# Kernel optimization log

Measured on AMD Instinct MI355X. Metric: run time of the kernel, lower is better.

The kernel has to match this reference:

```python
import jax, jax.numpy as jnp
import numpy as np

D = 256        # model_dim
E = 4          # num_experts
H = 8          # attention heads
L = 8          # layers
P = 4          # patch size
IMG = 128
B = 8
NUM_CLASSES = 10
T = (IMG // P) ** 2  # 1024 tokens


def _ln(x, g, b):
    mu = jnp.mean(x, -1, keepdims=True)
    var = jnp.mean((x - mu) ** 2, -1, keepdims=True)
    return (x - mu) * jax.lax.rsqrt(var + 1e-5) * g + b


def setup_inputs() -> dict:
    key = jax.random.key(0)
    ks = jax.random.split(key, 24)
    n = lambda k, s, sc=0.02: jax.random.normal(k, s, jnp.float32) * sc
    return {
        "x": jax.random.normal(ks[0], (B, 3, IMG, IMG), jnp.float32),
        "patch_w": n(ks[1], (D, 3, P, P), 0.1),
        "patch_b": n(ks[2], (D,), 0.01),
        "pos_emb": n(ks[3], (1, T, D), 0.02),
        "router_w": n(ks[4], (E, D), 0.05),
        "router_b": n(ks[5], (E,), 0.01),
        "ln1_g": jnp.ones((L, D), jnp.float32),
        "ln1_b": jnp.zeros((L, D), jnp.float32),
        "q_w": n(ks[6], (L, D, D), 0.05),
        "q_b": n(ks[7], (L, D), 0.01),
        "k_w": n(ks[8], (L, D, D), 0.05),
        "k_b": n(ks[9], (L, D), 0.01),
        "v_w": n(ks[10], (L, D, D), 0.05),
        "v_b": n(ks[11], (L, D), 0.01),
        "o_w": n(ks[12], (L, D, D), 0.05),
        "o_b": n(ks[13], (L, D), 0.01),
        "ln2_g": jnp.ones((L, D), jnp.float32),
        "ln2_b": jnp.zeros((L, D), jnp.float32),
        "l1_w": n(ks[14], (L, 4 * D, D), 0.05),
        "l1_b": n(ks[15], (L, 4 * D), 0.01),
        "l2_w": n(ks[16], (L, D, 4 * D), 0.05),
        "l2_b": n(ks[17], (L, D), 0.01),
        "head_w": n(ks[18], (NUM_CLASSES, D), 0.05),
        "head_b": n(ks[19], (NUM_CLASSES,), 0.01),
        "alpha": jnp.full((1,), 0.5, jnp.float32),
    }


def reference(x, patch_w, patch_b, pos_emb, router_w, router_b, ln1_g, ln1_b,
              q_w, q_b, k_w, k_b, v_w, v_b, o_w, o_b, ln2_g, ln2_b,
              l1_w, l1_b, l2_w, l2_b, head_w, head_b, alpha):
    b = x.shape[0]
    # patch embed: Conv2d(3, D, P, stride=P)
    h = jax.lax.conv_general_dilated(x, patch_w, (P, P), 'VALID',
                                     dimension_numbers=('NCHW', 'OIHW', 'NCHW'))
    h = h + patch_b[None, :, None, None]
    tok = h.reshape(b, D, -1).transpose(0, 2, 1) + pos_emb   # [B,T,D]
    t = tok.shape[1]
    n_per = t // E  # uniform capacity: floor(T * 1/E)
    raw_prob = jax.nn.softmax(tok @ router_w.T + router_b, axis=-1)  # [B,T,E]
    # greedy routing: expert e takes top n_per of remaining tokens, rows zeroed after
    prob = raw_prob
    bidx = jnp.arange(b)[:, None]
    blocks, pblocks = [], []
    for e in range(E):
        _, idx = jax.lax.top_k(prob[:, :, e], n_per)            # [B,n_per]
        blocks.append(jnp.take_along_axis(tok, idx[:, :, None], axis=1))
        pblocks.append(jnp.take_along_axis(raw_prob, idx[:, :, None], axis=1))
        sel = jnp.zeros((b, t), prob.dtype).at[bidx, idx].set(1.0)
        prob = prob * (1.0 - sel)[:, :, None]
    xs = jnp.concatenate(blocks, axis=1)    # [B,T,D] expert-sorted
    rp = jnp.concatenate(pblocks, axis=1)   # [B,T,E]

    widths = [D // 2 ** e for e in range(E)]  # [256,128,64,32]
    scale = D ** -0.5                         # note: model_dim, not head_dim
    dh = D // H
    for l in range(L):
        # ---- nested-expert MHSA ----
        xn = _ln(xs, ln1_g[l], ln1_b[l])
        qs, ks_, vs = [], [], []
        for e in range(E):
            m = widths[e]
            blk = xn[:, e * n_per:(e + 1) * n_per, :m]
            qs.append(blk @ q_w[l][:, :m].T + q_b[l])
            ks_.append(blk @ k_w[l][:, :m].T + k_b[l])
            vs.append(blk @ v_w[l][:, :m].T + v_b[l])
        q = jnp.concatenate(qs, 1).reshape(b, t, H, dh).transpose(0, 2, 1, 3)
        k = jnp.concatenate(ks_, 1).reshape(b, t, H, dh).transpose(0, 2, 1, 3)
        v = jnp.concatenate(vs, 1).reshape(b, t, H, dh).transpose(0, 2, 1, 3)
        attn = jax.nn.softmax(jnp.einsum('bhqd,bhkd->bhqk', q, k) * scale, axis=-1)
        ao = jnp.einsum('bhqk,bhkd->bhqd', attn, v).transpose(0, 2, 1, 3).reshape(b, t, D)
        outs = []
        for e in range(E):
            m = widths[e]
            sl = slice(e * n_per, (e + 1) * n_per)
            o = ao[:, sl, :m] @ o_w[l][:m, :m].T + o_b[l][:m]
            o = jnp.pad(o, ((0, 0), (0, 0), (0, D - m)))
            outs.append(o + xs[:, sl, :])
        xs = jnp.concatenate(outs, 1)
        # ---- nested-expert MLP ----
        xn = _ln(xs, ln2_g[l], ln2_b[l])
        outs = []
        for e in range(E):
            m = widths[e]
            sl = slice(e * n_per, (e + 1) * n_per)
            blk = xn[:, sl, :m]
            inner = jax.nn.gelu(blk @ l1_w[l][:, :m].T + l1_b[l], approximate=False)
            outer = inner @ l2_w[l][:m, :].T + l2_b[l][:m]
            outer = jnp.pad(outer, ((0, 0), (0, 0), (0, D - m)))
            sf = (alpha[0] * rp[:, sl, e] + 1.0)[:, :, None]
            outs.append(xs[:, sl, :] + sf * outer)
        xs = jnp.concatenate(outs, 1)
    # classification head: mean pool + linear
    return jnp.mean(xs, axis=1) @ head_w.T + head_b
```

## Files before the change

### kernel.cpp

```cpp
#include <hip/hip_runtime.h>
#include <math.h>

#define D 256
#define E 4
#define H 8
#define LYR 8
#define IMG 128
#define BB 8
#define NC 10
#define T 1024
#define NPER 256
#define DH 32
#define D4 1024

using bf16x8 = __attribute__((ext_vector_type(8))) __bf16;
using bf16x4 = __attribute__((ext_vector_type(4))) __bf16;
using f32x4  = __attribute__((ext_vector_type(4))) float;

#define MFMA16(a, b, c) __builtin_amdgcn_mfma_f32_16x16x32_bf16((a), (b), (c), 0, 0, 0)

__device__ __forceinline__ void gload16(const void* g, void* l) {
    __builtin_amdgcn_global_load_lds(
        (const __attribute__((address_space(1))) void*)g,
        (__attribute__((address_space(3))) void*)l, 16, 0, 0);
}

__global__ void cast6(const float* __restrict__ s0, const float* __restrict__ s1,
                      const float* __restrict__ s2, const float* __restrict__ s3,
                      const float* __restrict__ s4, const float* __restrict__ s5,
                      __bf16* __restrict__ d0, __bf16* __restrict__ d1,
                      __bf16* __restrict__ d2, __bf16* __restrict__ d3,
                      __bf16* __restrict__ d4, __bf16* __restrict__ d5) {
    const long A4 = (long)LYR * D * D / 4;
    const long W4 = (long)LYR * D4 * D / 4;
    long i = (long)blockIdx.x * 256 + threadIdx.x;
    const float* s; __bf16* d; long off;
    if (i < 4 * A4) {
        int w = (int)(i / A4); off = i - (long)w * A4;
        s = w == 0 ? s0 : w == 1 ? s1 : w == 2 ? s2 : s3;
        d = w == 0 ? d0 : w == 1 ? d1 : w == 2 ? d2 : d3;
    } else {
        long j = i - 4 * A4;
        int w = (int)(j / W4); off = j - (long)w * W4;
        s = w ? s5 : s4; d = w ? d5 : d4;
    }
    float4 v = ((const float4*)s)[off];
    bf16x4 o;
    o[0] = (__bf16)v.x; o[1] = (__bf16)v.y; o[2] = (__bf16)v.z; o[3] = (__bf16)v.w;
    ((bf16x4*)d)[off] = o;
}

__global__ void patch_router(const float* __restrict__ x, const float* __restrict__ pw,
                             const float* __restrict__ pb, const float* __restrict__ pos,
                             const float* __restrict__ rw, const float* __restrict__ rb,
                             float* __restrict__ tok, float* __restrict__ rawp) {
    int t = blockIdx.x, b = blockIdx.y, d = threadIdx.x;
    __shared__ float sx[48];
    __shared__ float srow[D];
    __shared__ float slog[4];
    int ph = t >> 5, pwc = t & 31;
    if (d < 48) {
        int c = d >> 4, ij = d & 15, i = ij >> 2, j = ij & 3;
        sx[d] = x[(((long)b * 3 + c) * IMG + (ph * 4 + i)) * IMG + (pwc * 4 + j)];
    }
    __syncthreads();
    float acc = pb[d];
    #pragma unroll
    for (int kk = 0; kk < 48; ++kk) acc += sx[kk] * pw[d * 48 + kk];
    float val = acc + pos[(long)t * D + d];
    tok[((long)b * T + t) * D + d] = val;
    srow[d] = val;
    __syncthreads();
    int wv = d >> 6, lane = d & 63;
    float a = 0.f;
    for (int c = lane; c < D; c += 64) a += srow[c] * rw[wv * D + c];
    for (int off = 32; off; off >>= 1) a += __shfl_down(a, off);
    if (lane == 0) slog[wv] = a + rb[wv];
    __syncthreads();
    if (d == 0) {
        float l0 = slog[0], l1 = slog[1], l2 = slog[2], l3 = slog[3];
        float mx = fmaxf(fmaxf(l0, l1), fmaxf(l2, l3));
        float e0 = __expf(l0 - mx), e1 = __expf(l1 - mx), e2 = __expf(l2 - mx), e3 = __expf(l3 - mx);
        float inv = 1.0f / (e0 + e1 + e2 + e3);
        long row = (long)b * T + t;
        rawp[row * 4 + 0] = e0 * inv;
        rawp[row * 4 + 1] = e1 * inv;
        rawp[row * 4 + 2] = e2 * inv;
        rawp[row * 4 + 3] = e3 * inv;
    }
}

__global__ __launch_bounds__(1024) void route_topk(const float* __restrict__ rawp,
                                                   int* __restrict__ perm,
                                                   float* __restrict__ rpsel) {
    int b = blockIdx.x, tid = threadIdx.x;
    int lane = tid & 63, wv = tid >> 6;
    __shared__ unsigned hist[256];
    __shared__ unsigned long long ball[16];
    __shared__ int sb_bin, sb_rem;
    bool assigned = false;
    for (int e = 0; e < E; ++e) {
        float v = rawp[((long)b * T + tid) * E + e];
        unsigned key = assigned ? 0u : __float_as_uint(v);
        unsigned prefix = 0;
        int rem = NPER;
        #pragma unroll
        for (int pass = 3; pass >= 0; --pass) {
            int shift = pass * 8;
            if (tid < 256) hist[tid] = 0;
            __syncthreads();
            bool active = (pass == 3) || ((key >> (shift + 8)) == prefix);
            if (active) atomicAdd(&hist[(key >> shift) & 255], 1u);
            __syncthreads();
            if (tid < 64) {
                unsigned c[4], psum = 0;
                #pragma unroll
                for (int u = 0; u < 4; ++u) { c[u] = hist[tid * 4 + u]; psum += c[u]; }
                unsigned suf = psum;
                #pragma unroll
                for (int off = 1; off < 64; off <<= 1) {
                    unsigned o = __shfl_down(suf, off);
                    if (tid + off < 64) suf += o;
                }
                unsigned El = suf - psum;
                if (El < (unsigned)rem && (unsigned)rem <= suf) {
                    unsigned cab = El;
                    #pragma unroll
                    for (int u = 3; u >= 0; --u) {
                        if ((unsigned)rem > cab && (unsigned)rem <= cab + c[u]) {
                            sb_bin = tid * 4 + u;
                            sb_rem = (int)((unsigned)rem - cab);
                        }
                        cab += c[u];
                    }
                }
            }
            __syncthreads();
            prefix = (prefix << 8) | (unsigned)sb_bin;
            rem = sb_rem;
        }
        unsigned t = prefix;
        bool is_tie = (!assigned) && (key == t);
        unsigned long long mbt = __ballot(is_tie);
        if (lane == 0) ball[wv] = mbt;
        __syncthreads();
        int tierank = 0;
        for (int w2 = 0; w2 < wv; ++w2) tierank += __popcll(ball[w2]);
        tierank += __popcll(mbt & ((1ULL << lane) - 1));
        bool sel = (!assigned) && ((key > t) || (is_tie && tierank < rem));
        __syncthreads();
        unsigned long long mbs = __ballot(sel);
        if (lane == 0) ball[wv] = mbs;
        __syncthreads();
        int rank = 0;
        for (int w2 = 0; w2 < wv; ++w2) rank += __popcll(ball[w2]);
        rank += __popcll(mbs & ((1ULL << lane) - 1));
        if (sel) {
            perm[(long)b * T + e * NPER + rank] = tid;
            rpsel[(long)b * T + e * NPER + rank] = v;
            assigned = true;
        }
        __syncthreads();
    }
}

__global__ void gather_tokens(const float* __restrict__ tok, const int* __restrict__ perm,
                              float* __restrict__ xs) {
    int slot = blockIdx.x, b = blockIdx.y, d = threadIdx.x;
    int src = perm[(long)b * T + slot];
    xs[((long)b * T + slot) * D + d] = tok[((long)b * T + src) * D + d];
}

__device__ __forceinline__ void ln_rows32(const float* __restrict__ src,
                                          const float* __restrict__ g,
                                          const float* __restrict__ bta,
                                          __bf16 (*slds)[264], int tid) {
    int sub = tid & 15, rowh = tid >> 4;
    int col0 = sub * 16;
    float gv[16], bv[16];
    #pragma unroll
    for (int u = 0; u < 4; ++u) {
        float4 gg = *(const float4*)&g[col0 + 4 * u];
        float4 bb = *(const float4*)&bta[col0 + 4 * u];
        gv[4*u] = gg.x; gv[4*u+1] = gg.y; gv[4*u+2] = gg.z; gv[4*u+3] = gg.w;
        bv[4*u] = bb.x; bv[4*u+1] = bb.y; bv[4*u+2] = bb.z; bv[4*u+3] = bb.w;
    }
    #pragma unroll
    for (int half = 0; half < 2; ++half) {
        int r = rowh + half * 16;
        const float* rp = src + (long)r * D + col0;
        float v[16];
        #pragma unroll
        for (int u = 0; u < 4; ++u) {
            float4 vv = *(const float4*)&rp[4 * u];
            v[4*u] = vv.x; v[4*u+1] = vv.y; v[4*u+2] = vv.z; v[4*u+3] = vv.w;
        }
        float s = 0.f;
        #pragma unroll
        for (int u = 0; u < 16; ++u) s += v[u];
        #pragma unroll
        for (int mk = 1; mk < 16; mk <<= 1) s += __shfl_xor(s, mk);
        float mu = s * (1.0f / D);
        float s2 = 0.f;
        #pragma unroll
        for (int u = 0; u < 16; ++u) { v[u] -= mu; s2 += v[u] * v[u]; }
        #pragma unroll
        for (int mk = 1; mk < 16; mk <<= 1) s2 += __shfl_xor(s2, mk);
        float rstd = rsqrtf(s2 * (1.0f / D) + 1e-5f);
        bf16x8 o0, o1;
        #pragma unroll
        for (int u = 0; u < 8; ++u) o0[u] = (__bf16)(v[u] * rstd * gv[u] + bv[u]);
        #pragma unroll
        for (int u = 0; u < 8; ++u) o1[u] = (__bf16)(v[8+u] * rstd * gv[8+u] + bv[8+u]);
        *(bf16x8*)&slds[r][col0]     = o0;
        *(bf16x8*)&slds[r][col0 + 8] = o1;
    }
}

template<int RG, int K>
__device__ __forceinline__ void gemm_tile(
    const __bf16* __restrict__ A, int lda,
    const __bf16* __restrict__ W, int ldb,
    int lane, f32x4 (&acc)[RG][4])
{
    int lr = lane & 15, lk = (lane >> 4) * 8;
    const __bf16* a0 = A + (long)lr * lda + lk;
    const __bf16* b0 = W + (long)lr * ldb + lk;
    const __bf16* b1 = b0 + 16 * ldb;
    const __bf16* b2 = b0 + 32 * ldb;
    const __bf16* b3 = b0 + 48 * ldb;
    constexpr int CH = (K <= 256) ? K : 128;
    for (int kb = 0; kb < K; kb += CH) {
        #pragma unroll
        for (int ku = 0; ku < CH; ku += 32) {
            int k = kb + ku;
            bf16x8 av[RG];
            #pragma unroll
            for (int i = 0; i < RG; ++i) av[i] = *(const bf16x8*)(a0 + i * 16 * lda + k);
            bf16x8 bv0 = *(const bf16x8*)(b0 + k);
            bf16x8 bv1 = *(const bf16x8*)(b1 + k);
            bf16x8 bv2 = *(const bf16x8*)(b2 + k);
            bf16x8 bv3 = *(const bf16x8*)(b3 + k);
            #pragma unroll
            for (int i = 0; i < RG; ++i) {
                acc[i][0] = MFMA16(av[i], bv0, acc[i][0]);
                acc[i][1] = MFMA16(av[i], bv1, acc[i][1]);
                acc[i][2] = MFMA16(av[i], bv2, acc[i][2]);
                acc[i][3] = MFMA16(av[i], bv3, acc[i][3]);
            }
        }
    }
}

#define GEMM_K_DISPATCH(RG, Aexpr, lda, Wexpr, ldb, accv)                        \
    switch (m) {                                                                 \
      case 256: gemm_tile<RG, 256>(Aexpr, lda, Wexpr, ldb, lane, accv); break;   \
      case 128: gemm_tile<RG, 128>(Aexpr, lda, Wexpr, ldb, lane, accv); break;   \
      case 64:  gemm_tile<RG, 64>(Aexpr, lda, Wexpr, ldb, lane, accv); break;    \
      default:  gemm_tile<RG, 32>(Aexpr, lda, Wexpr, ldb, lane, accv); break;    \
    }

__device__ __forceinline__ void tile_map(int tau, int& e, int& rt, int& ct) {
    if (tau < 64)       { e = 0; rt = tau >> 2; ct = tau & 3; }
    else if (tau < 96)  { e = 1; int t2 = tau - 64; rt = t2 >> 1; ct = t2 & 1; }
    else if (tau < 112) { e = 2; rt = tau - 96;  ct = 0; }
    else                { e = 3; rt = tau - 112; ct = 0; }
}

__global__ __launch_bounds__(256) void qkv_ln_gemm(
    const float* __restrict__ xs,
    const __bf16* __restrict__ qwb, const __bf16* __restrict__ kwb, const __bf16* __restrict__ vwb,
    const float* __restrict__ qb, const float* __restrict__ kb, const float* __restrict__ vb,
    const float* __restrict__ g, const float* __restrict__ bta,
    __bf16* __restrict__ Qb, __bf16* __restrict__ Kb, __bf16* __restrict__ Vt)
{
    int tid = threadIdx.x, lane = tid & 63, wid = tid >> 6;
    int tile = blockIdx.x, which = blockIdx.y, b = blockIdx.z;
    int row0 = tile * 32;
    int m = D >> (row0 >> 8);
    __shared__ __bf16 slds[32][264];
    ln_rows32(xs + ((long)b * T + row0) * D, g, bta, slds, tid);
    __syncthreads();
    const __bf16* W = which == 0 ? qwb : which == 1 ? kwb : vwb;
    const float* bias = which == 0 ? qb : which == 1 ? kb : vb;
    int ncol0 = wid * 64;
    const f32x4 vz = {0.f, 0.f, 0.f, 0.f};
    f32x4 acc[2][4];
    #pragma unroll
    for (int i = 0; i < 2; ++i) { acc[i][0]=vz; acc[i][1]=vz; acc[i][2]=vz; acc[i][3]=vz; }
    GEMM_K_DISPATCH(2, &slds[0][0], 264, W + (long)ncol0 * D, D, acc)
    int lr = lane & 15, rg = (lane >> 4) * 4;
    #pragma unroll
    for (int i = 0; i < 2; ++i) {
        int row = row0 + i * 16 + rg;
        #pragma unroll
        for (int j = 0; j < 4; ++j) {
            int n = ncol0 + j * 16 + lr;
            float bvs = bias[n];
            if (which == 2) {
                bf16x4 pk;
                #pragma unroll
                for (int r = 0; r < 4; ++r) pk[r] = (__bf16)(acc[i][j][r] + bvs);
                *(bf16x4*)&Vt[((long)b * D + n) * T + row] = pk;
            } else if (which == 0) {
                #pragma unroll
                for (int r = 0; r < 4; ++r)
                    Qb[((long)b * T + row + r) * D + n] = (__bf16)((acc[i][j][r] + bvs) * 0.0625f);
            } else {
                #pragma unroll
                for (int r = 0; r < 4; ++r)
                    Kb[((long)b * T + row + r) * D + n] = (__bf16)(acc[i][j][r] + bvs);
            }
        }
    }
}

__global__ __launch_bounds__(128) void attn_mfma(
    const __bf16* __restrict__ Qb, const __bf16* __restrict__ Kb,
    const __bf16* __restrict__ Vt, __bf16* __restrict__ aob)
{
    int bid = blockIdx.x;
    int bh = (bid & 7) * 8 + ((bid >> 3) & 7);
    int qt = bid >> 6;
    int b = bh >> 3, h = bh & 7;
    int tid = threadIdx.x;
    int lane = tid & 63, wave = tid >> 6;
    int lr = lane & 15, g = lane >> 4;
    int q0 = qt * 64 + wave * 32;
    __shared__ __bf16 plds[2][32][72];
    __shared__ __bf16 sK[2][4 * 64 * 8];
    __shared__ __bf16 sV[2][4 * 64 * 8];
    const f32x4 vz = {0.f, 0.f, 0.f, 0.f};
    bf16x8 qf[2];
    qf[0] = *(const bf16x8*)&Qb[((long)b * T + q0 + lr) * D + h * DH + g * 8];
    qf[1] = *(const bf16x8*)&Qb[((long)b * T + q0 + 16 + lr) * D + h * DH + g * 8];
    f32x4 acc[2][2] = {{vz, vz}, {vz, vz}};
    float ls[2] = {0.f, 0.f};
    int j0 = 2 * wave, j1 = 2 * wave + 1;
    const __bf16* kseg0 = Kb + ((long)b * T + 16 * j0 + lr) * D + h * DH + g * 8;
    const __bf16* kseg1 = Kb + ((long)b * T + 16 * j1 + lr) * D + h * DH + g * 8;
    const __bf16* vseg0 = Vt + ((long)b * D + h * DH + (j0 >> 1) * 16 + lr) * T
                             + 32 * (j0 & 1) + 8 * g;
    const __bf16* vseg1 = Vt + ((long)b * D + h * DH + (j1 >> 1) * 16 + lr) * T
                             + 32 * (j1 & 1) + 8 * g;

#define STAGE(BSEL, KC)                                        \
    {                                                          \
        gload16(kseg0 + (long)(KC) * D, &sK[BSEL][j0 * 512]);  \
        gload16(kseg1 + (long)(KC) * D, &sK[BSEL][j1 * 512]);  \
        gload16(vseg0 + (KC),           &sV[BSEL][j0 * 512]);  \
        gload16(vseg1 + (KC),           &sV[BSEL][j1 * 512]);  \
    }

#define COMPUTE(BSEL)                                                                     \
    {                                                                                     \
        bf16x8 kf[4], vf[2][2];                                                           \
        _Pragma("unroll")                                                                 \
        for (int j = 0; j < 4; ++j)                                                       \
            kf[j] = *(const bf16x8*)&sK[BSEL][(j * 64 + lane) * 8];                       \
        _Pragma("unroll")                                                                 \
        for (int w2 = 0; w2 < 2; ++w2)                                                    \
            _Pragma("unroll")                                                             \
            for (int df = 0; df < 2; ++df)                                                \
                vf[w2][df] = *(const bf16x8*)&sV[BSEL][((df * 2 + w2) * 64 + lane) * 8];  \
        _Pragma("unroll")                                                                 \
        for (int qi = 0; qi < 2; ++qi) {                                                  \
            _Pragma("unroll")                                                             \
            for (int j = 0; j < 4; ++j) {                                                 \
                f32x4 s = MFMA16(kf[j], qf[qi], vz);                                      \
                float p0 = __expf(s[0]), p1 = __expf(s[1]);                               \
                float p2 = __expf(s[2]), p3 = __expf(s[3]);                               \
                ls[qi] += (p0 + p1) + (p2 + p3);                                          \
                bf16x4 pk;                                                                \
                pk[0] = (__bf16)p0; pk[1] = (__bf16)p1;                                   \
                pk[2] = (__bf16)p2; pk[3] = (__bf16)p3;                                   \
                *(bf16x4*)&plds[wave][qi * 16 + lr][16 * j + 4 * g] = pk;                 \
            }                                                                             \
        }                                                                                 \
        _Pragma("unroll")                                                                 \
        for (int qi = 0; qi < 2; ++qi) {                                                  \
            _Pragma("unroll")                                                             \
            for (int w2 = 0; w2 < 2; ++w2) {                                              \
                bf16x8 pa = *(const bf16x8*)&plds[wave][qi * 16 + lr][32 * w2 + 8 * g];   \
                acc[qi][0] = MFMA16(pa, vf[w2][0], acc[qi][0]);                           \
                acc[qi][1] = MFMA16(pa, vf[w2][1], acc[qi][1]);                           \
            }                                                                             \
        }                                                                                 \
    }

    STAGE(0, 0)
    __syncthreads();
    int bsel = 0;
    for (int kc = 0; kc < T; kc += 64) {
        if (kc + 64 < T) STAGE(bsel ^ 1, kc + 64)
        COMPUTE(bsel)
        __syncthreads();
        bsel ^= 1;
    }
#undef STAGE
#undef COMPUTE

    #pragma unroll
    for (int qi = 0; qi < 2; ++qi) {
        ls[qi] += __shfl_xor(ls[qi], 16);
        ls[qi] += __shfl_xor(ls[qi], 32);
        float inv = 1.0f / ls[qi];
        #pragma unroll
        for (int r = 0; r < 4; ++r) {
            float invr = __shfl(inv, 4 * g + r);
            long obase = ((long)b * T + q0 + qi * 16 + 4 * g + r) * D + h * DH;
            aob[obase + lr]      = (__bf16)(acc[qi][0][r] * invr);
            aob[obase + 16 + lr] = (__bf16)(acc[qi][1][r] * invr);
        }
    }
}

__global__ __launch_bounds__(256) void oproj_gemm(
    const __bf16* __restrict__ aob, const __bf16* __restrict__ owb,
    const float* __restrict__ ob, float* __restrict__ xs)
{
    int tid = threadIdx.x, lane = tid & 63, wid = tid >> 6;
    int gw = blockIdx.x * 4 + wid;
    int b = gw >> 7, tau = gw & 127;
    int e, rt, ct;
    tile_map(tau, e, rt, ct);
    int m = D >> e;
    int row0 = e * NPER + rt * 16;
    int ncol0 = ct * 64;
    const f32x4 vz = {0.f, 0.f, 0.f, 0.f};
    f32x4 acc[1][4] = {{vz, vz, vz, vz}};
    GEMM_K_DISPATCH(1, aob + ((long)b * T + row0) * D, D, owb + (long)ncol0 * D, D, acc)
    int lr = lane & 15, rg = (lane >> 4) * 4;
    int row = row0 + rg;
    #pragma unroll
    for (int j = 0; j < 4; ++j) {
        int n = ncol0 + j * 16 + lr;
        if (n < m) {
            float bv = ob[n];
            #pragma unroll
            for (int r = 0; r < 4; ++r)
                xs[((long)b * T + row + r) * D + n] += acc[0][j][r] + bv;
        }
    }
}

__global__ __launch_bounds__(256) void mlp1_ln_gemm(
    const float* __restrict__ xs, const __bf16* __restrict__ w1b,
    const float* __restrict__ b1, const float* __restrict__ g, const float* __restrict__ bta,
    __bf16* __restrict__ innerb)
{
    int tid = threadIdx.x, lane = tid & 63, wid = tid >> 6;
    int tile = blockIdx.x, fq = blockIdx.y, b = blockIdx.z;
    int row0 = tile * 32;
    int m = D >> (row0 >> 8);
    __shared__ __bf16 slds[32][264];
    ln_rows32(xs + ((long)b * T + row0) * D, g, bta, slds, tid);
    __syncthreads();
    int ncol0 = fq * 256 + wid * 64;
    const f32x4 vz = {0.f, 0.f, 0.f, 0.f};
    f32x4 acc[2][4];
    #pragma unroll
    for (int i = 0; i < 2; ++i) { acc[i][0]=vz; acc[i][1]=vz; acc[i][2]=vz; acc[i][3]=vz; }
    GEMM_K_DISPATCH(2, &slds[0][0], 264, w1b + (long)ncol0 * D, D, acc)
    int lr = lane & 15, rg = (lane >> 4) * 4;
    #pragma unroll
    for (int i = 0; i < 2; ++i) {
        int row = row0 + i * 16 + rg;
        #pragma unroll
        for (int j = 0; j < 4; ++j) {
            int f = ncol0 + j * 16 + lr;
            float bv = b1[f];
            #pragma unroll
            for (int r = 0; r < 4; ++r) {
                float xv = acc[i][j][r] + bv;
                float gl = 0.5f * xv * (1.0f + erff(xv * 0.70710678118654752f));
                innerb[((long)b * T + row + r) * D4 + f] = (__bf16)gl;
            }
        }
    }
}

__global__ __launch_bounds__(256) void mlp2_gemm(
    const __bf16* __restrict__ innerb, const __bf16* __restrict__ w2b,
    const float* __restrict__ b2, const float* __restrict__ rpsel,
    const float* __restrict__ alpha, float* __restrict__ xs)
{
    int tid = threadIdx.x, lane = tid & 63, wid = tid >> 6;
    int gw = blockIdx.x * 4 + wid;
    int b = gw >> 7, tau = gw & 127;
    int e, rt, ct;
    tile_map(tau, e, rt, ct);
    int m = D >> e;
    int row0 = e * NPER + rt * 16;
    int ncol0 = ct * 64;
    const f32x4 vz = {0.f, 0.f, 0.f, 0.f};
    f32x4 acc[1][4] = {{vz, vz, vz, vz}};
    gemm_tile<1, 1024>(innerb + ((long)b * T + row0) * D4, D4,
                       w2b + (long)ncol0 * D4, D4, lane, acc);
    int lr = lane & 15, rg = (lane >> 4) * 4;
    int row = row0 + rg;
    float a0 = alpha[0];
    float sf[4];
    #pragma unroll
    for (int r = 0; r < 4; ++r) sf[r] = a0 * rpsel[(long)b * T + row + r] + 1.0f;
    #pragma unroll
    for (int j = 0; j < 4; ++j) {
        int n = ncol0 + j * 16 + lr;
        if (n < m) {
            float bv = b2[n];
            #pragma unroll
            for (int r = 0; r < 4; ++r)
                xs[((long)b * T + row + r) * D + n] += sf[r] * (acc[0][j][r] + bv);
        }
    }
}

__global__ void head_partial(const float* __restrict__ xs, float* __restrict__ part) {
    int c = blockIdx.x, b = blockIdx.y, d = threadIdx.x;
    const float* p = xs + ((long)b * T + c * 128) * D + d;
    float s = 0.f;
    #pragma unroll 8
    for (int i = 0; i < 128; ++i) s += p[(long)i * D];
    part[((long)b * 8 + c) * D + d] = s;
}

__global__ void head_final(const float* __restrict__ part, const float* __restrict__ hw,
                           const float* __restrict__ hb, float* __restrict__ out) {
    int b = blockIdx.x, d = threadIdx.x;
    __shared__ float smean[D];
    float s = 0.f;
    #pragma unroll
    for (int c = 0; c < 8; ++c) s += part[((long)b * 8 + c) * D + d];
    smean[d] = s * (1.0f / T);
    __syncthreads();
    if (d < NC) {
        float acc = hb[d];
        for (int c = 0; c < D; ++c) acc += smean[c] * hw[d * D + c];
        out[b * NC + d] = acc;
    }
}

extern "C" void kernel_launch(void* const* d_in, const int* in_sizes, int n_in,
                              void* d_out, int out_size, void* d_ws, size_t ws_size,
                              hipStream_t stream) {
    const float* x      = (const float*)d_in[0];
    const float* patchw = (const float*)d_in[1];
    const float* patchb = (const float*)d_in[2];
    const float* pos    = (const float*)d_in[3];
    const float* rw     = (const float*)d_in[4];
    const float* rb     = (const float*)d_in[5];
    const float* ln1g   = (const float*)d_in[6];
    const float* ln1b   = (const float*)d_in[7];
    const float* qw     = (const float*)d_in[8];
    const float* qbi    = (const float*)d_in[9];
    const float* kw     = (const float*)d_in[10];
    const float* kbi    = (const float*)d_in[11];
    const float* vw     = (const float*)d_in[12];
    const float* vbi    = (const float*)d_in[13];
    const float* ow     = (const float*)d_in[14];
    const float* obi    = (const float*)d_in[15];
    const float* ln2g   = (const float*)d_in[16];
    const float* ln2b   = (const float*)d_in[17];
    const float* l1w    = (const float*)d_in[18];
    const float* l1b    = (const float*)d_in[19];
    const float* l2w    = (const float*)d_in[20];
    const float* l2b    = (const float*)d_in[21];
    const float* hw     = (const float*)d_in[22];
    const float* hb     = (const float*)d_in[23];
    const float* alpha  = (const float*)d_in[24];

    char* p = (char*)d_ws;
    auto alloc = [&](size_t bytes) { void* r = (void*)p; p += (bytes + 255) & ~(size_t)255; return r; };
    const long NTD = (long)BB * T * D;

    float*  tok    = (float*)alloc(NTD * 4);
    float*  xs     = (float*)alloc(NTD * 4);
    float*  rawp   = (float*)alloc((long)BB * T * E * 4);
    float*  rpsel  = (float*)alloc((long)BB * T * 4);
    int*    perm   = (int*)alloc((long)BB * T * 4);
    float*  part   = (float*)alloc((long)BB * 8 * D * 4);
    __bf16* Qb     = (__bf16*)alloc(NTD * 2);
    __bf16* Kb     = (__bf16*)alloc(NTD * 2);
    __bf16* Vt     = (__bf16*)alloc(NTD * 2);
    __bf16* aob    = (__bf16*)alloc(NTD * 2);
    __bf16* innerb = (__bf16*)alloc((long)BB * T * D4 * 2);
    __bf16* qwb    = (__bf16*)alloc((long)LYR * D * D * 2);
    __bf16* kwb    = (__bf16*)alloc((long)LYR * D * D * 2);
    __bf16* vwb    = (__bf16*)alloc((long)LYR * D * D * 2);
    __bf16* owb    = (__bf16*)alloc((long)LYR * D * D * 2);
    __bf16* w1b    = (__bf16*)alloc((long)LYR * D4 * D * 2);
    __bf16* w2b    = (__bf16*)alloc((long)LYR * D * D4 * 2);

    cast6<<<6144, 256, 0, stream>>>(qw, kw, vw, ow, l1w, l2w, qwb, kwb, vwb, owb, w1b, w2b);

    patch_router<<<dim3(T, BB), 256, 0, stream>>>(x, patchw, patchb, pos, rw, rb, tok, rawp);
    route_topk<<<BB, 1024, 0, stream>>>(rawp, perm, rpsel);
    gather_tokens<<<dim3(T, BB), 256, 0, stream>>>(tok, perm, xs);

    for (int l = 0; l < LYR; ++l) {
        qkv_ln_gemm<<<dim3(32, 3, BB), 256, 0, stream>>>(
            xs, qwb + (long)l * D * D, kwb + (long)l * D * D, vwb + (long)l * D * D,
            qbi + l * D, kbi + l * D, vbi + l * D,
            ln1g + l * D, ln1b + l * D, Qb, Kb, Vt);
        attn_mfma<<<dim3(1024), 128, 0, stream>>>(Qb, Kb, Vt, aob);
        oproj_gemm<<<dim3(256), 256, 0, stream>>>(
            aob, owb + (long)l * D * D, obi + l * D, xs);
        mlp1_ln_gemm<<<dim3(32, 4, BB), 256, 0, stream>>>(
            xs, w1b + (long)l * D4 * D, l1b + (long)l * D4,
            ln2g + l * D, ln2b + l * D, innerb);
        mlp2_gemm<<<dim3(256), 256, 0, stream>>>(
            innerb, w2b + (long)l * D * D4, l2b + l * D, rpsel, alpha, xs);
    }

    head_partial<<<dim3(8, BB), 256, 0, stream>>>(xs, part);
    head_final<<<BB, D, 0, stream>>>(part, hw, hb, (float*)d_out);
}
```

Before: 905.8 us.

## Split attention query tile across four waves and use exp2 with folded scale

The attention kernel now runs 256 threads per block, so each of four waves handles 16 queries instead of two waves handling 32. K/V staging is spread across all four waves, one load each. Softmax switches from __expf to exp2, with log2(e) folded into the Q scaling constant written by the QKV GEMM. This aims to raise occupancy and latency hiding and to make the exponential cheaper. In exchange, each wave reuses its K/V LDS fragments for only 16 queries instead of 32, and the block has more threads to synchronise.

```diff
diff --git a/kernel.cpp b/kernel.cpp
--- a/kernel.cpp
+++ b/kernel.cpp
@@ -18,6 +18,7 @@
 using f32x4  = __attribute__((ext_vector_type(4))) float;
 
 #define MFMA16(a, b, c) __builtin_amdgcn_mfma_f32_16x16x32_bf16((a), (b), (c), 0, 0, 0)
+#define EXP2F(x) __builtin_exp2f(x)
 
 __device__ __forceinline__ void gload16(const void* g, void* l) {
     __builtin_amdgcn_global_load_lds(
@@ -305,7 +306,8 @@
             } else if (which == 0) {
                 #pragma unroll
                 for (int r = 0; r < 4; ++r)
-                    Qb[((long)b * T + row + r) * D + n] = (__bf16)((acc[i][j][r] + bvs) * 0.0625f);
+                    Qb[((long)b * T + row + r) * D + n] =
+                        (__bf16)((acc[i][j][r] + bvs) * 0.09016994375f);
             } else {
                 #pragma unroll
                 for (int r = 0; r < 4; ++r)
@@ -315,7 +317,7 @@
     }
 }
 
-__global__ __launch_bounds__(128) void attn_mfma(
+__global__ __launch_bounds__(256) void attn_mfma(
     const __bf16* __restrict__ Qb, const __bf16* __restrict__ Kb,
     const __bf16* __restrict__ Vt, __bf16* __restrict__ aob)
 {
@@ -326,30 +328,22 @@
     int tid = threadIdx.x;
     int lane = tid & 63, wave = tid >> 6;
     int lr = lane & 15, g = lane >> 4;
-    int q0 = qt * 64 + wave * 32;
-    __shared__ __bf16 plds[2][32][72];
+    int q0 = qt * 64 + wave * 16;
+    __shared__ __bf16 plds[4][16][72];
     __shared__ __bf16 sK[2][4 * 64 * 8];
     __shared__ __bf16 sV[2][4 * 64 * 8];
     const f32x4 vz = {0.f, 0.f, 0.f, 0.f};
-    bf16x8 qf[2];
-    qf[0] = *(const bf16x8*)&Qb[((long)b * T + q0 + lr) * D + h * DH + g * 8];
-    qf[1] = *(const bf16x8*)&Qb[((long)b * T + q0 + 16 + lr) * D + h * DH + g * 8];
-    f32x4 acc[2][2] = {{vz, vz}, {vz, vz}};
-    float ls[2] = {0.f, 0.f};
-    int j0 = 2 * wave, j1 = 2 * wave + 1;
-    const __bf16* kseg0 = Kb + ((long)b * T + 16 * j0 + lr) * D + h * DH + g * 8;
-    const __bf16* kseg1 = Kb + ((long)b * T + 16 * j1 + lr) * D + h * DH + g * 8;
-    const __bf16* vseg0 = Vt + ((long)b * D + h * DH + (j0 >> 1) * 16 + lr) * T
-                             + 32 * (j0 & 1) + 8 * g;
-    const __bf16* vseg1 = Vt + ((long)b * D + h * DH + (j1 >> 1) * 16 + lr) * T
-                             + 32 * (j1 & 1) + 8 * g;
+    bf16x8 qf = *(const bf16x8*)&Qb[((long)b * T + q0 + lr) * D + h * DH + g * 8];
+    f32x4 acc0 = vz, acc1 = vz;
+    float ls = 0.f;
+    const __bf16* kseg = Kb + ((long)b * T + 16 * wave + lr) * D + h * DH + g * 8;
+    const __bf16* vseg = Vt + ((long)b * D + h * DH + (wave >> 1) * 16 + lr) * T
+                            + 32 * (wave & 1) + 8 * g;
 
 #define STAGE(BSEL, KC)                                        \
     {                                                          \
-        gload16(kseg0 + (long)(KC) * D, &sK[BSEL][j0 * 512]);  \
-        gload16(kseg1 + (long)(KC) * D, &sK[BSEL][j1 * 512]);  \
-        gload16(vseg0 + (KC),           &sV[BSEL][j0 * 512]);  \
-        gload16(vseg1 + (KC),           &sV[BSEL][j1 * 512]);  \
+        gload16(kseg + (long)(KC) * D, &sK[BSEL][wave * 512]); \
+        gload16(vseg + (KC),           &sV[BSEL][wave * 512]); \
     }
 
 #define COMPUTE(BSEL)                                                                     \
@@ -364,27 +358,21 @@
             for (int df = 0; df < 2; ++df)                                                \
                 vf[w2][df] = *(const bf16x8*)&sV[BSEL][((df * 2 + w2) * 64 + lane) * 8];  \
         _Pragma("unroll")                                                                 \
-        for (int qi = 0; qi < 2; ++qi) {                                                  \
-            _Pragma("unroll")                                                             \
-            for (int j = 0; j < 4; ++j) {                                                 \
-                f32x4 s = MFMA16(kf[j], qf[qi], vz);                                      \
-                float p0 = __expf(s[0]), p1 = __expf(s[1]);                               \
-                float p2 = __expf(s[2]), p3 = __expf(s[3]);                               \
-                ls[qi] += (p0 + p1) + (p2 + p3);                                          \
-                bf16x4 pk;                                                                \
-                pk[0] = (__bf16)p0; pk[1] = (__bf16)p1;                                   \
-                pk[2] = (__bf16)p2; pk[3] = (__bf16)p3;                                   \
-                *(bf16x4*)&plds[wave][qi * 16 + lr][16 * j + 4 * g] = pk;                 \
-            }                                                                             \
+        for (int j = 0; j < 4; ++j) {                                                     \
+            f32x4 s = MFMA16(kf[j], qf, vz);      \
+            float p0 = EXP2F(s[0]), p1 = EXP2F(s[1]);                                     \
+            float p2 = EXP2F(s[2]), p3 = EXP2F(s[3]);                                     \
+            ls += (p0 + p1) + (p2 + p3);                                                  \
+            bf16x4 pk;                                                                    \
+            pk[0] = (__bf16)p0; pk[1] = (__bf16)p1;                                       \
+            pk[2] = (__bf16)p2; pk[3] = (__bf16)p3;                                       \
+            *(bf16x4*)&plds[wave][lr][16 * j + 4 * g] = pk;                               \
         }                                                                                 \
         _Pragma("unroll")                                                                 \
-        for (int qi = 0; qi < 2; ++qi) {                                                  \
-            _Pragma("unroll")                                                             \
-            for (int w2 = 0; w2 < 2; ++w2) {                                              \
-                bf16x8 pa = *(const bf16x8*)&plds[wave][qi * 16 + lr][32 * w2 + 8 * g];   \
-                acc[qi][0] = MFMA16(pa, vf[w2][0], acc[qi][0]);                           \
-                acc[qi][1] = MFMA16(pa, vf[w2][1], acc[qi][1]);                           \
-            }                                                                             \
+        for (int w2 = 0; w2 < 2; ++w2) {                                                  \
+            bf16x8 pa = *(const bf16x8*)&plds[wave][lr][32 * w2 + 8 * g];                 \
+            acc0 = MFMA16(pa, vf[w2][0], acc0);                                           \
+            acc1 = MFMA16(pa, vf[w2][1], acc1);                                           \
         }                                                                                 \
     }
 
@@ -400,18 +388,15 @@
 #undef STAGE
 #undef COMPUTE
 
-    #pragma unroll
-    for (int qi = 0; qi < 2; ++qi) {
-        ls[qi] += __shfl_xor(ls[qi], 16);
-        ls[qi] += __shfl_xor(ls[qi], 32);
-        float inv = 1.0f / ls[qi];
-        #pragma unroll
-        for (int r = 0; r < 4; ++r) {
-            float invr = __shfl(inv, 4 * g + r);
-            long obase = ((long)b * T + q0 + qi * 16 + 4 * g + r) * D + h * DH;
-            aob[obase + lr]      = (__bf16)(acc[qi][0][r] * invr);
-            aob[obase + 16 + lr] = (__bf16)(acc[qi][1][r] * invr);
-        }
+    ls += __shfl_xor(ls, 16);
+    ls += __shfl_xor(ls, 32);
+    float inv = 1.0f / ls;
+    #pragma unroll
+    for (int r = 0; r < 4; ++r) {
+        float invr = __shfl(inv, 4 * g + r);
+        long obase = ((long)b * T + q0 + 4 * g + r) * D + h * DH;
+        aob[obase + lr]      = (__bf16)(acc0[r] * invr);
+        aob[obase + 16 + lr] = (__bf16)(acc1[r] * invr);
     }
 }
 
@@ -602,7 +587,7 @@
             xs, qwb + (long)l * D * D, kwb + (long)l * D * D, vwb + (long)l * D * D,
             qbi + l * D, kbi + l * D, vbi + l * D,
             ln1g + l * D, ln1b + l * D, Qb, Kb, Vt);
-        attn_mfma<<<dim3(1024), 128, 0, stream>>>(Qb, Kb, Vt, aob);
+        attn_mfma<<<dim3(1024), 256, 0, stream>>>(Qb, Kb, Vt, aob);
         oproj_gemm<<<dim3(256), 256, 0, stream>>>(
             aob, owb + (long)l * D * D, obi + l * D, xs);
         mlp1_ln_gemm<<<dim3(32, 4, BB), 256, 0, stream>>>(
```

Result: slower. 1.181 ms (+30.4%).
